# Optimization experiments

Hardware: AMD Instinct MI355X
Metric: run time of the kernel (lower is better)

Reference implementation:

```python
import jax, jax.numpy as jnp
import numpy as np

N = 786432   # total points (batch of ~4 LiDAR scans)
U = 131072   # occupied voxels
FEA_DIM = 9
EPS = 1e-5


def _bn_params(key, c):
    k1, k2, k3, k4 = jax.random.split(key, 4)
    g = 1.0 + 0.1 * jax.random.normal(k1, (c,), jnp.float32)
    b = 0.1 * jax.random.normal(k2, (c,), jnp.float32)
    m = 0.1 * jax.random.normal(k3, (c,), jnp.float32)
    v = jax.random.uniform(k4, (c,), jnp.float32, 0.5, 1.5)
    return jnp.stack([g, b, m, v])  # [4, c]


def _linear(key, fin, fout):
    kw, kb = jax.random.split(key)
    w = jax.random.normal(kw, (fin, fout), jnp.float32) / np.sqrt(fin)
    b = 0.01 * jax.random.normal(kb, (fout,), jnp.float32)
    return w, b


def setup_inputs() -> dict:
    key = jax.random.key(0)
    ks = jax.random.split(key, 12)
    cat_pt_fea = jax.random.normal(ks[0], (N, FEA_DIM), jnp.float32)
    occupy = (jax.random.uniform(ks[1], (N, 1)) < 0.9).astype(jnp.float32)
    # voxel coords [batch_idx, 3 cyl inds]; values arbitrary ints (metadata only)
    unq = jax.random.randint(ks[2], (U, 4), 0, 480, dtype=jnp.int32)
    # inverse map point->voxel, guaranteeing every voxel is hit at least once
    unq_inv = jnp.concatenate([
        jnp.arange(U, dtype=jnp.int32),
        jax.random.randint(ks[3], (N - U,), 0, U, dtype=jnp.int32)])
    bn0 = _bn_params(ks[4], FEA_DIM)
    w1, b1 = _linear(ks[5], FEA_DIM, 64)
    bn2 = _bn_params(ks[6], 64)
    w2, b2 = _linear(ks[7], 64, 128)
    bn5 = _bn_params(ks[8], 128)
    w3, b3 = _linear(ks[9], 128, 256)
    bn8 = _bn_params(ks[10], 256)
    w4, b4 = _linear(jax.random.fold_in(key, 100), 256, 256)
    wc, bc = _linear(ks[11], 256, 16)
    return dict(cat_pt_fea=cat_pt_fea, occupy=occupy, unq=unq, unq_inv=unq_inv,
                bn0=bn0, w1=w1, b1=b1, bn2=bn2, w2=w2, b2=b2, bn5=bn5,
                w3=w3, b3=b3, bn8=bn8, w4=w4, b4=b4, wc=wc, bc=bc)


def _bn(x, p):
    g, b, m, v = p[0], p[1], p[2], p[3]
    return (x - m) * (g * jax.lax.rsqrt(v + EPS)) + b


def reference(cat_pt_fea, occupy, unq, unq_inv, bn0, w1, b1, bn2, w2, b2,
              bn5, w3, b3, bn8, w4, b4, wc, bc):
    # per-point PointNet MLP with occupy masking after BN/Linear layers
    x = _bn(cat_pt_fea, bn0) * occupy
    x = (x @ w1 + b1) * occupy
    x = _bn(x, bn2) * occupy
    x = jax.nn.relu(x)
    x = (x @ w2 + b2) * occupy
    x = _bn(x, bn5) * occupy
    x = jax.nn.relu(x)
    x = (x @ w3 + b3) * occupy
    x = _bn(x, bn8) * occupy
    x = jax.nn.relu(x)
    x = (x @ w4 + b4) * occupy                       # [N, 256]
    num_vox = unq.shape[0]
    pooled = jax.ops.segment_max(x, unq_inv, num_segments=num_vox)  # [U, 256]
    # occupy of the max-index point per voxel (mirrors scatter_max on arange)
    unq_idx = jax.ops.segment_max(jnp.arange(unq_inv.shape[0]), unq_inv,
                                  num_segments=num_vox)
    pooled_occupy = occupy[unq_idx]                  # [U, 1]
    out = jax.nn.relu(pooled @ wc + bc) * pooled_occupy  # fea_compression
    return unq, out, pooled_occupy
```

## Files before the change

### kernel.cpp

```cpp
#include <hip/hip_runtime.h>

#define N_PTS 786432
#define U_VOX 131072
#define NBLK  (N_PTS/64)

typedef __attribute__((ext_vector_type(8))) short v8s;
typedef __attribute__((ext_vector_type(4))) float v4f;

__device__ __forceinline__ unsigned short f2bf(float x){
    unsigned u = __float_as_uint(x);
    u += 0x7fffu + ((u >> 16) & 1u);
    return (unsigned short)(u >> 16);
}
__device__ __forceinline__ unsigned cvtpk(float lo, float hi){
    unsigned r;
    asm("v_cvt_pk_bf16_f32 %0, %1, %2" : "=v"(r) : "v"(lo), "v"(hi));
    return r;
}

__global__ __launch_bounds__(256) void k_fold(
    const float* __restrict__ bn0, const float* __restrict__ w1,
    const float* __restrict__ b1,  const float* __restrict__ bn2,
    const float* __restrict__ w2,  const float* __restrict__ b2,
    const float* __restrict__ bn5, const float* __restrict__ w3,
    const float* __restrict__ b3,  const float* __restrict__ bn8,
    const float* __restrict__ w4,  const float* __restrict__ wc,
    float* __restrict__ b1ff, float* __restrict__ b2f, float* __restrict__ b3f,
    unsigned short* __restrict__ wp1, unsigned short* __restrict__ wp2,
    unsigned short* __restrict__ wp3, unsigned short* __restrict__ wp4,
    unsigned short* __restrict__ wcp)
{
    __shared__ float s0[9],t0[9],s2[64],t2[64],s5[128],t5[128],s8[256],t8[256];
    int tid = threadIdx.x;
    if (tid < 9){  float g=bn0[tid], b=bn0[9+tid],  m=bn0[18+tid],  v=bn0[27+tid];
        float s=g*rsqrtf(v+1e-5f); s0[tid]=s; t0[tid]=b-m*s; }
    if (tid < 64){ float g=bn2[tid], b=bn2[64+tid], m=bn2[128+tid], v=bn2[192+tid];
        float s=g*rsqrtf(v+1e-5f); s2[tid]=s; t2[tid]=b-m*s; }
    if (tid < 128){float g=bn5[tid], b=bn5[128+tid],m=bn5[256+tid], v=bn5[384+tid];
        float s=g*rsqrtf(v+1e-5f); s5[tid]=s; t5[tid]=b-m*s; }
    { float g=bn8[tid], b=bn8[256+tid], m=bn8[512+tid], v=bn8[768+tid];
        float s=g*rsqrtf(v+1e-5f); s8[tid]=s; t8[tid]=b-m*s; }
    __syncthreads();
    if (blockIdx.x == 0){
        if (tid < 64){ float a=0.f;
            for (int k=0;k<9;k++) a += t0[k]*w1[k*64+tid];
            b1ff[tid]=(a+b1[tid])*s2[tid]+t2[tid]; }
        if (tid<128) b2f[tid]=b2[tid]*s5[tid]+t5[tid];
        b3f[tid]=b3[tid]*s8[tid]+t8[tid];
    }
    const int g0 = blockIdx.x*256 + tid, gstep = 32*256;
    for (int e=g0;e<2048;e+=gstep){
        int i=e&7, l=(e>>3)&63, jt=(e>>9)&3;
        int k=((l>>4)<<3)+i, j=jt*16+(l&15);
        wp1[e] = (k<9) ? f2bf(s0[k]*w1[k*64+j]*s2[j]) : (unsigned short)0;
    }
    for (int e=g0;e<8192;e+=gstep){
        int i=e&7, l=(e>>3)&63, jt=(e>>9)&7, ks=(e>>12)&1;
        int k=ks*32+((l>>4)<<3)+i, j=jt*16+(l&15);
        wp2[e]=f2bf(w2[k*128+j]*s5[j]);
    }
    for (int e=g0;e<32768;e+=gstep){
        int i=e&7, l=(e>>3)&63, jt=(e>>9)&15, ks=e>>13;
        int k=ks*32+((l>>4)<<3)+i, j=jt*16+(l&15);
        wp3[e]=f2bf(w3[k*256+j]*s8[j]);
    }
    for (int e=g0;e<65536;e+=gstep){
        int i=e&7, l=(e>>3)&63, jt=(e>>9)&15, ks=e>>13;
        int k=ks*32+((l>>4)<<3)+i, j=jt*16+(l&15);
        wp4[e]=f2bf(w4[k*256+j]);
    }
    for (int e=g0;e<4096;e+=gstep){
        int i=e&7, l=(e>>3)&63, ks=e>>9;
        int k=ks*32+((l>>4)<<3)+i, j=l&15;
        wcp[e]=f2bf(wc[k*16+j]);
    }
}

__global__ void k_hist(const int* __restrict__ uinv, int* __restrict__ cnt){
    int i=blockIdx.x*256+threadIdx.x;
    atomicAdd(cnt + uinv[i], 1);
}
__global__ void k_scan1(int* __restrict__ cnt, int* __restrict__ bsum){
    __shared__ int s[256];
    int t=threadIdx.x, i=blockIdx.x*256+t;
    int v=cnt[i]; s[t]=v; __syncthreads();
    for (int off=1;off<256;off<<=1){
        int x=(t>=off)?s[t-off]:0; __syncthreads();
        s[t]+=x; __syncthreads();
    }
    cnt[i]=s[t]-v;
    if (t==255) bsum[blockIdx.x]=s[255];
}
__global__ void k_scan2(int* __restrict__ bsum){
    __shared__ int s[512];
    int t=threadIdx.x;
    int v=bsum[t]; s[t]=v; __syncthreads();
    for (int off=1;off<512;off<<=1){
        int x=(t>=off)?s[t-off]:0; __syncthreads();
        s[t]+=x; __syncthreads();
    }
    bsum[t]=s[t]-v;
}
__global__ void k_scan3u(const int* __restrict__ cnt, const int* __restrict__ bsum,
                         int* __restrict__ cur,
                         const int* __restrict__ unq, float* __restrict__ outf){
    int i=blockIdx.x*256+threadIdx.x;
    cur[i]=cnt[i]+bsum[blockIdx.x];
    int4 u = *(const int4*)(unq + 4*i);
    *(float4*)(outf + 4*i) = make_float4((float)u.x,(float)u.y,(float)u.z,(float)u.w);
}
__global__ void k_scatgath(const int* __restrict__ uinv,
    const float* __restrict__ cat, const float* __restrict__ occ,
    int* __restrict__ cur, int* __restrict__ uidx,
    unsigned short* __restrict__ scat16, int* __restrict__ svoxS)
{
    int i = blockIdx.x*256 + threadIdx.x;
    int v = uinv[i];
    int slot = atomicAdd(cur + v, 1);
    atomicMax(uidx + v, i);
    const float* src = cat + (size_t)i*9;
    unsigned short tmp[16];
#pragma unroll
    for (int k=0;k<9;k++) tmp[k] = f2bf(src[k]);
    tmp[9] = f2bf(occ[i]);
#pragma unroll
    for (int k=10;k<16;k++) tmp[k]=0;
    uint4* dst = (uint4*)(scat16 + (size_t)slot*16);
    dst[0] = *(uint4*)(tmp);
    dst[1] = *(uint4*)(tmp+8);
    svoxS[slot] = v;
}

__global__ __launch_bounds__(256,4) void k_fused(
    const unsigned short* __restrict__ scat16g, const int* __restrict__ svoxS,
    const unsigned short* __restrict__ wp1, const float* __restrict__ b1ff,
    const unsigned short* __restrict__ wp2, const float* __restrict__ b2f,
    const unsigned short* __restrict__ wp3, const float* __restrict__ b3f,
    const unsigned short* __restrict__ wp4, const float* __restrict__ b4,
    unsigned* __restrict__ pooled, unsigned* __restrict__ bpool)
{
    __shared__ __align__(16) char smem[35344];
    int*   svox = (int*)smem;
    float* socc = (float*)(smem+256);
    int*   vpn  = (int*)(smem+512);
    float* pmlo = (float*)(smem+528);
    float* pmhi = (float*)(smem+1040);
    char*  R1   = smem + 1552;
    char*  sh1  = R1;
    char*  sh2  = R1 + 9216;

    const int tid = threadIdx.x;
    const int blk = blockIdx.x;
    const int p0  = blk*64;
    const int w = tid>>6, l = tid&63, lane16 = l&15, hi = l>>4;

    if (tid < 64) svox[tid] = svoxS[p0+tid];
    if (tid >= 64 && tid < 128){
        int t = tid-64;
        unsigned short ob = scat16g[(size_t)(p0+t)*16 + 9];
        socc[t] = __uint_as_float(((unsigned)ob)<<16);
    }
    if (tid==128) vpn[0] = (p0>0)        ? svoxS[p0-1]  : -1;
    if (tid==129) vpn[1] = (p0+64<N_PTS) ? svoxS[p0+64] : -1;

    {
        v4f bias = *(const v4f*)(b1ff + w*16 + 4*hi);
        v8s aw = *(const v8s*)(wp1 + (size_t)(w*64 + l)*8);
        const unsigned short* abase = scat16g + (size_t)p0*16 + hi*8;
#pragma unroll
        for (int mt=0;mt<4;mt++){
            v8s act = *(const v8s*)(abase + (mt*16+lane16)*16);
            v4f acc1 = __builtin_amdgcn_mfma_f32_16x16x32_bf16(aw, act, bias, 0,0,0);
            char* dst = sh1 + (mt*16+lane16)*144 + (w*16 + 4*hi)*2;
            *(unsigned*)(dst  ) = cvtpk(fmaxf(acc1[0],0.f), fmaxf(acc1[1],0.f));
            *(unsigned*)(dst+4) = cvtpk(fmaxf(acc1[2],0.f), fmaxf(acc1[3],0.f));
        }
    }
    __syncthreads();

    {
        v4f acc2[4][2];
#pragma unroll
        for (int jj=0;jj<2;jj++){
            v4f bias = *(const v4f*)(b2f + w*32 + jj*16 + 4*hi);
#pragma unroll
            for (int mt=0;mt<4;mt++) acc2[mt][jj]=bias;
        }
#pragma unroll
        for (int ks=0;ks<2;ks++){
            v8s a[4];
#pragma unroll
            for (int mt=0;mt<4;mt++)
                a[mt] = *(const v8s*)(sh1 + (mt*16+lane16)*144 + hi*16 + ks*64);
#pragma unroll
            for (int jj=0;jj<2;jj++){
                v8s bw = *(const v8s*)(wp2 + (size_t)((ks*8 + w*2 + jj)*64 + l)*8);
#pragma unroll
                for (int mt=0;mt<4;mt++)
                    acc2[mt][jj]=__builtin_amdgcn_mfma_f32_16x16x32_bf16(bw, a[mt], acc2[mt][jj],0,0,0);
            }
        }
#pragma unroll
        for (int mt=0;mt<4;mt++){
            char* dst = sh2 + (mt*16+lane16)*272;
#pragma unroll
            for (int jj=0;jj<2;jj++){
                int cb = (w*32 + jj*16 + 4*hi)*2;
                *(unsigned*)(dst+cb  ) = cvtpk(fmaxf(acc2[mt][jj][0],0.f), fmaxf(acc2[mt][jj][1],0.f));
                *(unsigned*)(dst+cb+4) = cvtpk(fmaxf(acc2[mt][jj][2],0.f), fmaxf(acc2[mt][jj][3],0.f));
            }
        }
    }
    __syncthreads();

    {
        v4f acc3[4][4];
#pragma unroll
        for (int jj=0;jj<4;jj++){
            v4f bias = *(const v4f*)(b3f + w*64 + jj*16 + 4*hi);
#pragma unroll
            for (int mt=0;mt<4;mt++) acc3[mt][jj]=bias;
        }
#pragma unroll
        for (int ks=0;ks<4;ks++){
            v8s a[4];
#pragma unroll
            for (int mt=0;mt<4;mt++)
                a[mt] = *(const v8s*)(sh2 + (mt*16+lane16)*272 + hi*16 + ks*64);
#pragma unroll
            for (int jj=0;jj<4;jj++){
                v8s bw = *(const v8s*)(wp3 + (size_t)((ks*16 + w*4 + jj)*64 + l)*8);
#pragma unroll
                for (int mt=0;mt<4;mt++)
                    acc3[mt][jj]=__builtin_amdgcn_mfma_f32_16x16x32_bf16(bw, a[mt], acc3[mt][jj],0,0,0);
            }
        }
        __syncthreads();
#pragma unroll
        for (int mt=0;mt<4;mt++){
            char* dst = R1 + (mt*16+lane16)*528;
#pragma unroll
            for (int jj=0;jj<4;jj++){
                int cb = (w*64 + jj*16 + 4*hi)*2;
                *(unsigned*)(dst+cb  ) = cvtpk(fmaxf(acc3[mt][jj][0],0.f), fmaxf(acc3[mt][jj][1],0.f));
                *(unsigned*)(dst+cb+4) = cvtpk(fmaxf(acc3[mt][jj][2],0.f), fmaxf(acc3[mt][jj][3],0.f));
            }
        }
    }
    __syncthreads();

    {
        v4f acc4[4][4];
#pragma unroll
        for (int jj=0;jj<4;jj++){
            v4f bias = *(const v4f*)(b4 + w*64 + jj*16 + 4*hi);
#pragma unroll
            for (int mt=0;mt<4;mt++) acc4[mt][jj]=bias;
        }
#pragma unroll
        for (int ks=0;ks<8;ks++){
            v8s a[4];
#pragma unroll
            for (int mt=0;mt<4;mt++)
                a[mt] = *(const v8s*)(R1 + (mt*16+lane16)*528 + hi*16 + ks*64);
#pragma unroll
            for (int jj=0;jj<4;jj++){
                v8s bw = *(const v8s*)(wp4 + (size_t)((ks*16 + w*4 + jj)*64 + l)*8);
#pragma unroll
                for (int mt=0;mt<4;mt++)
                    acc4[mt][jj]=__builtin_amdgcn_mfma_f32_16x16x32_bf16(bw, a[mt], acc4[mt][jj],0,0,0);
            }
        }
        __syncthreads();
#pragma unroll
        for (int mt=0;mt<4;mt++){
            int P = mt*16 + lane16;
            char* dst = R1 + P*528;
            float oc = socc[P];
#pragma unroll
            for (int jj=0;jj<4;jj++){
                int cb = (w*64 + jj*16 + 4*hi)*2;
                *(unsigned*)(dst+cb  ) = cvtpk(acc4[mt][jj][0]*oc, acc4[mt][jj][1]*oc);
                *(unsigned*)(dst+cb+4) = cvtpk(acc4[mt][jj][2]*oc, acc4[mt][jj][3]*oc);
            }
        }
    }
    __syncthreads();

    {
        const int half = tid>>7, c = tid&127, rb = half*32;
        int vl = svox[l];
        int vln = (l<63)? svox[l+1] : (int)0x80000000;
        unsigned long long mask = __ballot((l==63) || (vl!=vln));
        const int vp0=vpn[0], vp1=vpn[1];
        const bool cross = (svox[31]==svox[32]);
        float m0=-3.0e38f, m1=-3.0e38f, d0=0.f, d1=0.f;
        int segStart = rb, dEnd = 0; bool defer=false;
#pragma unroll 8
        for (int k=0;k<32;k++){
            int r = rb + k;
            unsigned x = *(const unsigned*)(R1 + r*528 + c*4);
            m0 = fmaxf(m0, __uint_as_float(x<<16));
            m1 = fmaxf(m1, __uint_as_float(x & 0xFFFF0000u));
            if ((mask>>r)&1ull){
                int v = svox[r];
                if (half==1 && segStart==32 && cross){
                    defer=true; d0=m0; d1=m1; dEnd=r;
                } else {
                    bool bp = (segStart==0) && (v==vp0);
                    bool bn = (r==63) && (v==vp1);
                    unsigned pk = cvtpk(m0,m1);
                    if (bp) bpool[((size_t)blk*2+0)*128 + c] = pk;
                    if (bn) bpool[((size_t)blk*2+1)*128 + c] = pk;
                    if (!bp && !bn) pooled[(size_t)v*128 + c] = pk;
                }
                m0=-3.0e38f; m1=-3.0e38f; segStart=r+1;
            }
        }
        if (half==0 && !((mask>>31)&1ull)){ pmlo[c]=m0; pmhi[c]=m1; }
        __syncthreads();
        if (defer){
            m0 = fmaxf(d0, pmlo[c]); m1 = fmaxf(d1, pmhi[c]);
            unsigned long long lowm = mask & 0x7FFFFFFFull;
            int ts = lowm ? (64 - __clzll(lowm)) : 0;
            int v = svox[32];
            bool bp = (ts==0) && (v==vp0);
            bool bn = (dEnd==63) && (v==vp1);
            unsigned pk = cvtpk(m0,m1);
            if (bp) bpool[((size_t)blk*2+0)*128 + c] = pk;
            if (bn) bpool[((size_t)blk*2+1)*128 + c] = pk;
            if (!bp && !bn) pooled[(size_t)v*128 + c] = pk;
        }
    }
}

__global__ __launch_bounds__(256) void k_bmerge(
    const int* __restrict__ cnt, const int* __restrict__ bsum,
    const int* __restrict__ cur, const unsigned* __restrict__ bpool,
    unsigned* __restrict__ pooled)
{
    int tid = threadIdx.x;
    int c = tid & 127, vv = tid>>7;
    int base = blockIdx.x*16 + vv*8;
#pragma unroll
    for (int i=0;i<8;i++){
        int v = base + i;
        int start = cnt[v] + bsum[v>>8];
        int end   = cur[v];
        int bs = start>>6, be = (end-1)>>6;
        if (bs==be) continue;
        unsigned x = bpool[((size_t)bs*2+1)*128 + c];
        float m0 = __uint_as_float(x<<16);
        float m1 = __uint_as_float(x & 0xFFFF0000u);
        for (int b=bs+1;b<be;b++){
            unsigned y = bpool[((size_t)b*2+1)*128 + c];
            m0 = fmaxf(m0, __uint_as_float(y<<16));
            m1 = fmaxf(m1, __uint_as_float(y & 0xFFFF0000u));
        }
        unsigned z = bpool[((size_t)be*2+0)*128 + c];
        m0 = fmaxf(m0, __uint_as_float(z<<16));
        m1 = fmaxf(m1, __uint_as_float(z & 0xFFFF0000u));
        pooled[(size_t)v*128 + c] = cvtpk(m0,m1);
    }
}

__global__ __launch_bounds__(256) void k_head(
    const unsigned short* __restrict__ pooled16,
    const unsigned short* __restrict__ wcp, const float* __restrict__ bc,
    const float* __restrict__ occ, const int* __restrict__ uidx,
    float* __restrict__ outf)
{
    __shared__ float pocc[64];
    int tid=threadIdx.x;
    int v0 = blockIdx.x*64;
    if (tid<64){
        float p = occ[uidx[v0+tid]];
        pocc[tid]=p;
        outf[2621440 + v0 + tid] = p;
    }
    __syncthreads();
    int w=tid>>6, l=tid&63, lane16=l&15, hi=l>>4;
    int vb = w*16;
    float bcj = bc[lane16];
    v4f acc = {bcj,bcj,bcj,bcj};
#pragma unroll
    for (int ks=0;ks<8;ks++){
        v8s a = *(const v8s*)(pooled16 + (size_t)(v0 + vb + lane16)*256 + ks*32 + hi*8);
        v8s b = *(const v8s*)(wcp + (size_t)(ks*64 + l)*8);
        acc = __builtin_amdgcn_mfma_f32_16x16x32_bf16(a, b, acc, 0,0,0);
    }
#pragma unroll
    for (int r=0;r<4;r++){
        int vx = vb + 4*hi + r;
        outf[524288 + (size_t)(v0+vx)*16 + lane16] = fmaxf(acc[r],0.f) * pocc[vx];
    }
}

extern "C" void kernel_launch(void* const* d_in, const int* in_sizes, int n_in,
                              void* d_out, int out_size, void* d_ws, size_t ws_size,
                              hipStream_t stream)
{
    const float* cat =(const float*)d_in[0];
    const float* occ =(const float*)d_in[1];
    const int*   unq =(const int*)  d_in[2];
    const int*   uinv=(const int*)  d_in[3];
    const float* bn0 =(const float*)d_in[4];
    const float* w1  =(const float*)d_in[5];
    const float* b1  =(const float*)d_in[6];
    const float* bn2 =(const float*)d_in[7];
    const float* w2  =(const float*)d_in[8];
    const float* b2  =(const float*)d_in[9];
    const float* bn5 =(const float*)d_in[10];
    const float* w3  =(const float*)d_in[11];
    const float* b3  =(const float*)d_in[12];
    const float* bn8 =(const float*)d_in[13];
    const float* w4  =(const float*)d_in[14];
    const float* b4  =(const float*)d_in[15];
    const float* wc  =(const float*)d_in[16];
    const float* bc  =(const float*)d_in[17];

    char* ws = (char*)d_ws;
    unsigned*       pooled = (unsigned*)ws;
    unsigned short* scat16 = (unsigned short*)(ws + 67108864);
    int*            svoxS  = (int*)(ws + 92274688);
    unsigned*       bpool  = (unsigned*)(ws + 95420416);
    int*            cnt    = (int*)(ws + 108003328);
    int*            uidx   = (int*)(ws + 108527616);
    int*            cur    = (int*)(ws + 109051904);
    int*            bsum   = (int*)(ws + 109576192);
    float*          b1ff   = (float*)(ws + 109578240);
    float*          b2f    = (float*)(ws + 109578496);
    float*          b3f    = (float*)(ws + 109579008);
    unsigned short* wp1    = (unsigned short*)(ws + 109580032);
    unsigned short* wp2    = (unsigned short*)(ws + 109584128);
    unsigned short* wp3    = (unsigned short*)(ws + 109600512);
    unsigned short* wp4    = (unsigned short*)(ws + 109666048);
    unsigned short* wcp    = (unsigned short*)(ws + 109797120);

    float* outf = (float*)d_out;

    hipMemsetAsync((void*)cnt, 0, 1048576, stream);
    k_fold    <<<32,        256,0,stream>>>(bn0,w1,b1,bn2,w2,b2,bn5,w3,b3,bn8,w4,wc,
                                            b1ff,b2f,b3f,wp1,wp2,wp3,wp4,wcp);
    k_hist    <<<N_PTS/256, 256,0,stream>>>(uinv,cnt);
    k_scan1   <<<U_VOX/256, 256,0,stream>>>(cnt,bsum);
    k_scan2   <<<1,         512,0,stream>>>(bsum);
    k_scan3u  <<<U_VOX/256, 256,0,stream>>>(cnt,bsum,cur,unq,outf);
    k_scatgath<<<N_PTS/256, 256,0,stream>>>(uinv,cat,occ,cur,uidx,scat16,svoxS);
    k_fused   <<<NBLK,      256,0,stream>>>(scat16,svoxS,wp1,b1ff,wp2,b2f,
                                            wp3,b3f,wp4,b4,pooled,bpool);
    k_bmerge  <<<U_VOX/16,  256,0,stream>>>(cnt,bsum,cur,bpool,pooled);
    k_head    <<<U_VOX/64,  256,0,stream>>>((unsigned short*)pooled,wcp,bc,occ,uidx,outf);
}
```

Before: 343.8 us.

## Fuse three-pass scan into single-pass decoupled lookback scan and stage inputs in LDS

Replaces the three scan kernels with one kernel that uses a decoupled lookback scheme over per-block flags, removing two launches and the separate bsum pass. The fused MLP kernel now stages each block's input rows into shared memory with coalesced 16-byte loads before the first MFMA, and the bf16 stores are widened to 8 bytes. The lookback relies on blocks making forward progress in order and on flags being zeroed by the enlarged memset.

```diff
diff --git a/kernel.cpp b/kernel.cpp
--- a/kernel.cpp
+++ b/kernel.cpp
@@ -80,34 +80,39 @@
     int i=blockIdx.x*256+threadIdx.x;
     atomicAdd(cnt + uinv[i], 1);
 }
-__global__ void k_scan1(int* __restrict__ cnt, int* __restrict__ bsum){
+__global__ __launch_bounds__(256) void k_scan(
+    int* __restrict__ cnt, int* __restrict__ cur, unsigned* __restrict__ bflag,
+    const int* __restrict__ unq, float* __restrict__ outf)
+{
     __shared__ int s[256];
-    int t=threadIdx.x, i=blockIdx.x*256+t;
+    __shared__ int sbase;
+    int b=blockIdx.x, t=threadIdx.x, i=b*256+t;
     int v=cnt[i]; s[t]=v; __syncthreads();
     for (int off=1;off<256;off<<=1){
         int x=(t>=off)?s[t-off]:0; __syncthreads();
         s[t]+=x; __syncthreads();
     }
-    cnt[i]=s[t]-v;
-    if (t==255) bsum[blockIdx.x]=s[255];
-}
-__global__ void k_scan2(int* __restrict__ bsum){
-    __shared__ int s[512];
-    int t=threadIdx.x;
-    int v=bsum[t]; s[t]=v; __syncthreads();
-    for (int off=1;off<512;off<<=1){
-        int x=(t>=off)?s[t-off]:0; __syncthreads();
-        s[t]+=x; __syncthreads();
-    }
-    bsum[t]=s[t]-v;
-}
-__global__ void k_scan3u(const int* __restrict__ cnt, const int* __restrict__ bsum,
-                         int* __restrict__ cur,
-                         const int* __restrict__ unq, float* __restrict__ outf){
-    int i=blockIdx.x*256+threadIdx.x;
-    cur[i]=cnt[i]+bsum[blockIdx.x];
+    if (t==255)
+        __hip_atomic_store(bflag+b, ((unsigned)s[255]<<2)|1u,
+                           __ATOMIC_RELEASE, __HIP_MEMORY_SCOPE_AGENT);
     int4 u = *(const int4*)(unq + 4*i);
     *(float4*)(outf + 4*i) = make_float4((float)u.x,(float)u.y,(float)u.z,(float)u.w);
+    if (t==0){
+        int base=0;
+        for (int p=b-1;p>=0;--p){
+            unsigned f;
+            do { f=__hip_atomic_load(bflag+p, __ATOMIC_ACQUIRE,
+                                     __HIP_MEMORY_SCOPE_AGENT); } while(!(f&3u));
+            base += (int)(f>>2);
+            if ((f&3u)==2u) break;
+        }
+        sbase=base;
+        __hip_atomic_store(bflag+b, ((unsigned)(base+s[255])<<2)|2u,
+                           __ATOMIC_RELEASE, __HIP_MEMORY_SCOPE_AGENT);
+    }
+    __syncthreads();
+    int e = sbase + s[t]-v;
+    cnt[i]=e; cur[i]=e;
 }
 __global__ void k_scatgath(const int* __restrict__ uinv,
     const float* __restrict__ cat, const float* __restrict__ occ,
@@ -146,34 +151,38 @@
     float* pmlo = (float*)(smem+528);
     float* pmhi = (float*)(smem+1040);
     char*  R1   = smem + 1552;
-    char*  sh1  = R1;
-    char*  sh2  = R1 + 9216;
+    unsigned short* inp = (unsigned short*)R1;
+    char*  sh1  = R1 + 3072;
+    char*  sh2  = R1 + 12288;
 
     const int tid = threadIdx.x;
     const int blk = blockIdx.x;
     const int p0  = blk*64;
     const int w = tid>>6, l = tid&63, lane16 = l&15, hi = l>>4;
 
-    if (tid < 64) svox[tid] = svoxS[p0+tid];
-    if (tid >= 64 && tid < 128){
-        int t = tid-64;
-        unsigned short ob = scat16g[(size_t)(p0+t)*16 + 9];
-        socc[t] = __uint_as_float(((unsigned)ob)<<16);
-    }
+    if (tid < 128){
+        int p = tid>>1, q = tid&1;
+        uint4 d = *(const uint4*)(scat16g + (size_t)p0*16 + tid*8);
+        *(uint4*)(inp + p*24 + q*8) = d;
+    }
+    if (tid < 64) svox[tid] = svoxS[p0 + tid];
     if (tid==128) vpn[0] = (p0>0)        ? svoxS[p0-1]  : -1;
     if (tid==129) vpn[1] = (p0+64<N_PTS) ? svoxS[p0+64] : -1;
+    __syncthreads();
+    if (tid < 64)
+        socc[tid] = __uint_as_float(((unsigned)inp[tid*24+9])<<16);
 
     {
         v4f bias = *(const v4f*)(b1ff + w*16 + 4*hi);
         v8s aw = *(const v8s*)(wp1 + (size_t)(w*64 + l)*8);
-        const unsigned short* abase = scat16g + (size_t)p0*16 + hi*8;
 #pragma unroll
         for (int mt=0;mt<4;mt++){
-            v8s act = *(const v8s*)(abase + (mt*16+lane16)*16);
+            int P = mt*16 + lane16;
+            v8s act = *(const v8s*)(inp + P*24 + hi*8);
             v4f acc1 = __builtin_amdgcn_mfma_f32_16x16x32_bf16(aw, act, bias, 0,0,0);
-            char* dst = sh1 + (mt*16+lane16)*144 + (w*16 + 4*hi)*2;
-            *(unsigned*)(dst  ) = cvtpk(fmaxf(acc1[0],0.f), fmaxf(acc1[1],0.f));
-            *(unsigned*)(dst+4) = cvtpk(fmaxf(acc1[2],0.f), fmaxf(acc1[3],0.f));
+            *(uint2*)(sh1 + P*144 + (w*16 + 4*hi)*2) = make_uint2(
+                cvtpk(fmaxf(acc1[0],0.f), fmaxf(acc1[1],0.f)),
+                cvtpk(fmaxf(acc1[2],0.f), fmaxf(acc1[3],0.f)));
         }
     }
     __syncthreads();
@@ -206,8 +215,9 @@
 #pragma unroll
             for (int jj=0;jj<2;jj++){
                 int cb = (w*32 + jj*16 + 4*hi)*2;
-                *(unsigned*)(dst+cb  ) = cvtpk(fmaxf(acc2[mt][jj][0],0.f), fmaxf(acc2[mt][jj][1],0.f));
-                *(unsigned*)(dst+cb+4) = cvtpk(fmaxf(acc2[mt][jj][2],0.f), fmaxf(acc2[mt][jj][3],0.f));
+                *(uint2*)(dst+cb) = make_uint2(
+                    cvtpk(fmaxf(acc2[mt][jj][0],0.f), fmaxf(acc2[mt][jj][1],0.f)),
+                    cvtpk(fmaxf(acc2[mt][jj][2],0.f), fmaxf(acc2[mt][jj][3],0.f)));
             }
         }
     }
@@ -242,8 +252,9 @@
 #pragma unroll
             for (int jj=0;jj<4;jj++){
                 int cb = (w*64 + jj*16 + 4*hi)*2;
-                *(unsigned*)(dst+cb  ) = cvtpk(fmaxf(acc3[mt][jj][0],0.f), fmaxf(acc3[mt][jj][1],0.f));
-                *(unsigned*)(dst+cb+4) = cvtpk(fmaxf(acc3[mt][jj][2],0.f), fmaxf(acc3[mt][jj][3],0.f));
+                *(uint2*)(dst+cb) = make_uint2(
+                    cvtpk(fmaxf(acc3[mt][jj][0],0.f), fmaxf(acc3[mt][jj][1],0.f)),
+                    cvtpk(fmaxf(acc3[mt][jj][2],0.f), fmaxf(acc3[mt][jj][3],0.f)));
             }
         }
     }
@@ -280,8 +291,9 @@
 #pragma unroll
             for (int jj=0;jj<4;jj++){
                 int cb = (w*64 + jj*16 + 4*hi)*2;
-                *(unsigned*)(dst+cb  ) = cvtpk(acc4[mt][jj][0]*oc, acc4[mt][jj][1]*oc);
-                *(unsigned*)(dst+cb+4) = cvtpk(acc4[mt][jj][2]*oc, acc4[mt][jj][3]*oc);
+                *(uint2*)(dst+cb) = make_uint2(
+                    cvtpk(acc4[mt][jj][0]*oc, acc4[mt][jj][1]*oc),
+                    cvtpk(acc4[mt][jj][2]*oc, acc4[mt][jj][3]*oc));
             }
         }
     }
@@ -292,6 +304,7 @@
         int vl = svox[l];
         int vln = (l<63)? svox[l+1] : (int)0x80000000;
         unsigned long long mask = __ballot((l==63) || (vl!=vln));
+        unsigned mh = (unsigned)(mask >> rb);
         const int vp0=vpn[0], vp1=vpn[1];
         const bool cross = (svox[31]==svox[32]);
         float m0=-3.0e38f, m1=-3.0e38f, d0=0.f, d1=0.f;
@@ -302,7 +315,7 @@
             unsigned x = *(const unsigned*)(R1 + r*528 + c*4);
             m0 = fmaxf(m0, __uint_as_float(x<<16));
             m1 = fmaxf(m1, __uint_as_float(x & 0xFFFF0000u));
-            if ((mask>>r)&1ull){
+            if ((mh>>k)&1u){
                 int v = svox[r];
                 if (half==1 && segStart==32 && cross){
                     defer=true; d0=m0; d1=m1; dEnd=r;
@@ -317,7 +330,7 @@
                 m0=-3.0e38f; m1=-3.0e38f; segStart=r+1;
             }
         }
-        if (half==0 && !((mask>>31)&1ull)){ pmlo[c]=m0; pmhi[c]=m1; }
+        if (half==0 && !((mh>>31)&1u)){ pmlo[c]=m0; pmhi[c]=m1; }
         __syncthreads();
         if (defer){
             m0 = fmaxf(d0, pmlo[c]); m1 = fmaxf(d1, pmhi[c]);
@@ -335,9 +348,8 @@
 }
 
 __global__ __launch_bounds__(256) void k_bmerge(
-    const int* __restrict__ cnt, const int* __restrict__ bsum,
-    const int* __restrict__ cur, const unsigned* __restrict__ bpool,
-    unsigned* __restrict__ pooled)
+    const int* __restrict__ cnt, const int* __restrict__ cur,
+    const unsigned* __restrict__ bpool, unsigned* __restrict__ pooled)
 {
     int tid = threadIdx.x;
     int c = tid & 127, vv = tid>>7;
@@ -345,7 +357,7 @@
 #pragma unroll
     for (int i=0;i<8;i++){
         int v = base + i;
-        int start = cnt[v] + bsum[v>>8];
+        int start = cnt[v];
         int end   = cur[v];
         int bs = start>>6, be = (end-1)>>6;
         if (bs==be) continue;
@@ -426,8 +438,8 @@
     unsigned*       bpool  = (unsigned*)(ws + 95420416);
     int*            cnt    = (int*)(ws + 108003328);
     int*            uidx   = (int*)(ws + 108527616);
-    int*            cur    = (int*)(ws + 109051904);
-    int*            bsum   = (int*)(ws + 109576192);
+    unsigned*       bflag  = (unsigned*)(ws + 109051904);
+    int*            cur    = (int*)(ws + 109053952);
     float*          b1ff   = (float*)(ws + 109578240);
     float*          b2f    = (float*)(ws + 109578496);
     float*          b3f    = (float*)(ws + 109579008);
@@ -439,16 +451,14 @@
 
     float* outf = (float*)d_out;
 
-    hipMemsetAsync((void*)cnt, 0, 1048576, stream);
+    hipMemsetAsync((void*)cnt, 0, 1050624, stream);
     k_fold    <<<32,        256,0,stream>>>(bn0,w1,b1,bn2,w2,b2,bn5,w3,b3,bn8,w4,wc,
                                             b1ff,b2f,b3f,wp1,wp2,wp3,wp4,wcp);
     k_hist    <<<N_PTS/256, 256,0,stream>>>(uinv,cnt);
-    k_scan1   <<<U_VOX/256, 256,0,stream>>>(cnt,bsum);
-    k_scan2   <<<1,         512,0,stream>>>(bsum);
-    k_scan3u  <<<U_VOX/256, 256,0,stream>>>(cnt,bsum,cur,unq,outf);
+    k_scan    <<<U_VOX/256, 256,0,stream>>>(cnt,cur,bflag,unq,outf);
     k_scatgath<<<N_PTS/256, 256,0,stream>>>(uinv,cat,occ,cur,uidx,scat16,svoxS);
     k_fused   <<<NBLK,      256,0,stream>>>(scat16,svoxS,wp1,b1ff,wp2,b2f,
                                             wp3,b3f,wp4,b4,pooled,bpool);
-    k_bmerge  <<<U_VOX/16,  256,0,stream>>>(cnt,bsum,cur,bpool,pooled);
+    k_bmerge  <<<U_VOX/16,  256,0,stream>>>(cnt,cur,bpool,pooled);
     k_head    <<<U_VOX/64,  256,0,stream>>>((unsigned short*)pooled,wcp,bc,occ,uidx,outf);
 }
```

New measurement: 494.0 us. +43.7%, slower.
